# Optimization experiments

Hardware: AMD Instinct MI355X
Metric: run time of the kernel (lower is better)

The kernel has to match this reference:

```python
import jax, jax.numpy as jnp
import numpy as np

N, NFEAT, NHID, NCLASS, NLAYERS = 10000, 512, 256, 40, 8
LAMDA, ALPHA = 0.5, 0.1
EDGE_P = 0.003  # avg degree ~30


def setup_inputs() -> dict:
    key = jax.random.key(0)
    ks = jax.random.split(key, 8)
    x = jax.random.normal(ks[0], (N, NFEAT), dtype=jnp.float32)
    # binary adjacency with zero diagonal (normalize_adj asserts diag==0)
    adj = (jax.random.uniform(ks[1], (N, N)) < EDGE_P).astype(jnp.float32)
    adj = adj * (1.0 - jnp.eye(N, dtype=jnp.float32))
    # GraphConvolution.reset_parameters: uniform(-1/sqrt(out), 1/sqrt(out))
    s = 1.0 / np.sqrt(NHID)
    conv_w = jax.random.uniform(ks[2], (NLAYERS, NHID, NHID), jnp.float32, -s, s)
    s0 = 1.0 / np.sqrt(NFEAT)
    w0 = jax.random.uniform(ks[3], (NFEAT, NHID), jnp.float32, -s0, s0)
    b0 = jax.random.uniform(ks[4], (NHID,), jnp.float32, -s0, s0)
    s1 = 1.0 / np.sqrt(NHID)
    w1 = jax.random.uniform(ks[5], (NHID, NCLASS), jnp.float32, -s1, s1)
    b1 = jax.random.uniform(ks[6], (NCLASS,), jnp.float32, -s1, s1)
    return {"x": x, "adj": adj, "w0": w0, "b0": b0, "conv_w": conv_w, "w1": w1, "b1": b1}


def reference(x, adj, w0, b0, conv_w, w1, b1):
    n = adj.shape[0]
    # normalize_adj: A_hat = A + I; D^{-1/2} A_hat D^{-1/2}
    a_hat = adj + jnp.eye(n, dtype=adj.dtype)
    d_inv_sqrt = jax.lax.rsqrt(jnp.sum(a_hat, axis=1))
    a_norm = a_hat * d_inv_sqrt[:, None] * d_inv_sqrt[None, :]

    # dropout is a no-op in eval mode
    h0 = jax.nn.relu(x @ w0 + b0)  # [N, NHID]
    thetas = jnp.log(LAMDA / jnp.arange(1, NLAYERS + 1, dtype=jnp.float32) + 1.0)

    def step(h, wt):
        w, theta = wt
        hi = a_norm @ h                              # aggregation
        support = (1.0 - ALPHA) * hi + ALPHA * h0    # initial-residual mix (variant=False: r = support)
        out = theta * (support @ w) + (1.0 - theta) * support
        return jax.nn.relu(out), None

    h, _ = jax.lax.scan(step, h0, (conv_w, thetas))
    logits = h @ w1 + b1  # [N, NCLASS]
    return jax.nn.log_softmax(logits, axis=1)
```

## Files before the change

kernel.cpp:

```cpp
#include <hip/hip_runtime.h>
#include <math.h>

#define NN 10000
#define NFEAT 512
#define NHID 256
#define NCLASS 40
#define NLAYERS 8
#define MAXDEG 96

#define CVX_BLOCKS 5000
#define PW_BLOCKS  2560
#define PE_BLOCKS  3750

typedef __attribute__((ext_vector_type(8))) short bf16x8;
typedef __attribute__((ext_vector_type(4))) float floatx4;
typedef __attribute__((ext_vector_type(2))) float floatx2;
typedef __attribute__((ext_vector_type(4))) unsigned short ushort4v;

__device__ __forceinline__ unsigned short f2bf(float f) {
    union { float f; unsigned int u; } v; v.f = f;
    unsigned int r = v.u + 0x7fffu + ((v.u >> 16) & 1u);
    return (unsigned short)(r >> 16);
}
__device__ __forceinline__ float bf2f(unsigned short h) {
    union { unsigned int u; float f; } v; v.u = ((unsigned int)h) << 16;
    return v.f;
}
__device__ __forceinline__ unsigned char f2fp8(float f) {
    return (unsigned char)(__builtin_amdgcn_cvt_pk_fp8_f32(f, f, 0, false) & 0xFF);
}

__global__ __launch_bounds__(256) void build_graph(const float* __restrict__ adj,
                                                   int* __restrict__ cnt,
                                                   int* __restrict__ ell,
                                                   float* __restrict__ dinv) {
    int i = blockIdx.x;
    __shared__ int scnt;
    if (threadIdx.x == 0) scnt = 0;
    __syncthreads();
    const float4* row = (const float4*)(adj + (size_t)i * NN);
    const int nv = NN / 4;
    int* erow = ell + (size_t)i * MAXDEG;
    for (int f = threadIdx.x; f < nv; f += 256) {
        float4 v = row[f];
        if (v.x != 0.0f) { int s = atomicAdd(&scnt, 1); if (s < MAXDEG) erow[s] = 4*f + 0; }
        if (v.y != 0.0f) { int s = atomicAdd(&scnt, 1); if (s < MAXDEG) erow[s] = 4*f + 1; }
        if (v.z != 0.0f) { int s = atomicAdd(&scnt, 1); if (s < MAXDEG) erow[s] = 4*f + 2; }
        if (v.w != 0.0f) { int s = atomicAdd(&scnt, 1); if (s < MAXDEG) erow[s] = 4*f + 3; }
    }
    __syncthreads();
    if (threadIdx.x == 0) {
        int c = scnt;
        cnt[i] = (c < MAXDEG) ? c : MAXDEG;
        dinv[i] = rsqrtf(1.0f + (float)c);
    }
}

__global__ __launch_bounds__(256) void prep_all(const float* __restrict__ x,
                                                unsigned short* __restrict__ xb,
                                                const float* __restrict__ w0,
                                                const float* __restrict__ cw,
                                                unsigned short* __restrict__ w0t,
                                                unsigned short* __restrict__ Mt,
                                                const int* __restrict__ ell,
                                                const int* __restrict__ cnt,
                                                const float* __restrict__ dinv,
                                                int2* __restrict__ es) {
    int b = blockIdx.x, t = threadIdx.x;
    if (b < CVX_BLOCKS) {
        int idx = b * 256 + t;
        float4 v = ((const float4*)x)[idx];
        ushort4v o;
        o.x = f2bf(v.x); o.y = f2bf(v.y); o.z = f2bf(v.z); o.w = f2bf(v.w);
        ((ushort4v*)xb)[idx] = o;
    } else if (b < CVX_BLOCKS + PW_BLOCKS) {
        int idx = (b - CVX_BLOCKS) * 256 + t;
        if (idx < 131072) {
            int n = idx >> 9, k = idx & 511;
            w0t[idx] = f2bf(w0[(size_t)k * 256 + n]);
        } else {
            int j = idx - 131072;
            int l = j >> 16;
            int r = j & 65535;
            int n = r >> 8, k = r & 255;
            float theta = logf(0.5f / (float)(l + 1) + 1.0f);
            float v = theta * cw[(size_t)l * 65536 + (size_t)k * 256 + n];
            if (k == n) v += 1.0f - theta;
            Mt[j] = f2bf(v);
        }
    } else {
        int idx = (b - CVX_BLOCKS - PW_BLOCKS) * 256 + t;
        if (idx >= NN * MAXDEG) return;
        int i = idx / MAXDEG, e = idx % MAXDEG;
        int2 v; v.x = 0; v.y = 0;
        if (e < cnt[i]) {
            int j = ell[idx];
            v.x = j; v.y = __float_as_int(dinv[j]);
        }
        es[idx] = v;
    }
}

__global__ __launch_bounds__(512, 4) void gemm0_mfma(const unsigned short* __restrict__ xb,
                                                     const unsigned short* __restrict__ w0t,
                                                     const float* __restrict__ b0,
                                                     unsigned short* __restrict__ h0b,
                                                     unsigned char* __restrict__ h8o) {
    int t = threadIdx.x, wv = t >> 6, lane = t & 63;
    int lrow = lane & 15, quad = lane >> 4;
    int r0 = blockIdx.x * 16;

    bf16x8 a[16];
    const unsigned short* arow = xb + (size_t)(r0 + lrow) * NFEAT + quad * 8;
    #pragma unroll
    for (int f = 0; f < 16; ++f)
        a[f] = *(const bf16x8*)(arow + f * 32);

    #pragma unroll 1
    for (int n = 0; n < 2; ++n) {
        int nt = wv * 2 + n;
        floatx4 acc = {0.f, 0.f, 0.f, 0.f};
        const unsigned short* wrow = w0t + (size_t)(nt * 16 + lrow) * NFEAT + quad * 8;
        #pragma unroll
        for (int f = 0; f < 16; ++f) {
            bf16x8 b = *(const bf16x8*)(wrow + f * 32);
            acc = __builtin_amdgcn_mfma_f32_16x16x32_bf16(a[f], b, acc, 0, 0, 0);
        }
        int col = nt * 16 + lrow;
        float bias = b0[col];
        #pragma unroll
        for (int r = 0; r < 4; ++r) {
            int row = r0 + quad * 4 + r;
            unsigned short bv = f2bf(fmaxf(acc[r] + bias, 0.f));
            h0b[(size_t)row * NHID + col] = bv;
            h8o[(size_t)row * NHID + col] = f2fp8(bf2f(bv));
        }
    }
}

__device__ __forceinline__ void load_hg(const int2* __restrict__ e0r,
                                        const int2* __restrict__ e1r,
                                        const unsigned int* __restrict__ h8,
                                        int lane, int base,
                                        unsigned int (&x0)[4], unsigned int (&x1)[4],
                                        float (&s0)[4], float (&s1)[4]) {
    #pragma unroll
    for (int u = 0; u < 4; ++u) {
        int2 p = e0r[base + u];
        int2 q = e1r[base + u];
        s0[u] = __int_as_float(p.y);
        s1[u] = __int_as_float(q.y);
        x0[u] = h8[(size_t)p.x * 64 + lane];
        x1[u] = h8[(size_t)q.x * 64 + lane];
    }
}

__device__ __forceinline__ void proc_hg(const unsigned int (&x0)[4],
                                        const unsigned int (&x1)[4],
                                        const float (&s0)[4], const float (&s1)[4],
                                        float4& a0, float4& a1) {
    #pragma unroll
    for (int u = 0; u < 4; ++u) {
        floatx2 lo = __builtin_amdgcn_cvt_pk_f32_fp8(x0[u], false);
        floatx2 hi = __builtin_amdgcn_cvt_pk_f32_fp8(x0[u], true);
        a0.x = fmaf(s0[u], lo.x, a0.x);
        a0.y = fmaf(s0[u], lo.y, a0.y);
        a0.z = fmaf(s0[u], hi.x, a0.z);
        a0.w = fmaf(s0[u], hi.y, a0.w);
        lo = __builtin_amdgcn_cvt_pk_f32_fp8(x1[u], false);
        hi = __builtin_amdgcn_cvt_pk_f32_fp8(x1[u], true);
        a1.x = fmaf(s1[u], lo.x, a1.x);
        a1.y = fmaf(s1[u], lo.y, a1.y);
        a1.z = fmaf(s1[u], hi.x, a1.z);
        a1.w = fmaf(s1[u], hi.y, a1.w);
    }
}

template<bool LAST>
__global__ __launch_bounds__(512, 6) void layer_fused(const unsigned int* __restrict__ h8,
                                                      const unsigned short* __restrict__ h0b,
                                                      const float* __restrict__ dinv,
                                                      const int* __restrict__ cnt,
                                                      const int2* __restrict__ es,
                                                      const unsigned short* __restrict__ Mt,
                                                      const float* __restrict__ w1,
                                                      const float* __restrict__ b1,
                                                      unsigned char* __restrict__ h8_out,
                                                      float* __restrict__ out) {
    __shared__ unsigned short supb[16][264];
    __shared__ float hs[LAST ? 16 * 264 : 4];

    int t = threadIdx.x;
    int wv = __builtin_amdgcn_readfirstlane(t >> 6);
    int lane = t & 63;
    int r0 = blockIdx.x * 16;

    int lr0 = wv * 2, lr1 = lr0 + 1;
    int i0 = r0 + lr0, i1 = r0 + lr1;

    unsigned int su0 = h8[(size_t)i0 * 64 + lane];
    unsigned int su1 = h8[(size_t)i1 * 64 + lane];
    ushort4v h0v0 = ((const ushort4v*)h0b)[(size_t)i0 * 64 + lane];
    ushort4v h0v1 = ((const ushort4v*)h0b)[(size_t)i1 * 64 + lane];

    float di0 = dinv[i0], di1 = dinv[i1];
    int dA = (cnt[i0] + 7) & ~7, dB = (cnt[i1] + 7) & ~7;
    int dm = dA > dB ? dA : dB;
    const int2* e0r = es + (size_t)i0 * MAXDEG;
    const int2* e1r = es + (size_t)i1 * MAXDEG;

    floatx2 slo = __builtin_amdgcn_cvt_pk_f32_fp8(su0, false);
    floatx2 shi = __builtin_amdgcn_cvt_pk_f32_fp8(su0, true);
    float4 a0, a1;
    a0.x = di0 * slo.x; a0.y = di0 * slo.y; a0.z = di0 * shi.x; a0.w = di0 * shi.y;
    slo = __builtin_amdgcn_cvt_pk_f32_fp8(su1, false);
    shi = __builtin_amdgcn_cvt_pk_f32_fp8(su1, true);
    a1.x = di1 * slo.x; a1.y = di1 * slo.y; a1.z = di1 * shi.x; a1.w = di1 * shi.y;

    unsigned int xA0[4], xA1[4], xB0[4], xB1[4];
    float sA0[4], sA1[4], sB0[4], sB1[4];
    int nh = dm >> 2;
    if (nh > 0) {
        load_hg(e0r, e1r, h8, lane, 0, xA0, xA1, sA0, sA1);
        bool useA = true;
        #pragma unroll 1
        for (int g = 1; g < nh; ++g) {
            if (useA) {
                load_hg(e0r, e1r, h8, lane, g << 2, xB0, xB1, sB0, sB1);
                proc_hg(xA0, xA1, sA0, sA1, a0, a1);
            } else {
                load_hg(e0r, e1r, h8, lane, g << 2, xA0, xA1, sA0, sA1);
                proc_hg(xB0, xB1, sB0, sB1, a0, a1);
            }
            useA = !useA;
        }
        if (useA) proc_hg(xA0, xA1, sA0, sA1, a0, a1);
        else      proc_hg(xB0, xB1, sB0, sB1, a0, a1);
    }

    ushort4v ob;
    ob.x = f2bf(0.9f * (di0 * a0.x) + 0.1f * bf2f(h0v0.x));
    ob.y = f2bf(0.9f * (di0 * a0.y) + 0.1f * bf2f(h0v0.y));
    ob.z = f2bf(0.9f * (di0 * a0.z) + 0.1f * bf2f(h0v0.z));
    ob.w = f2bf(0.9f * (di0 * a0.w) + 0.1f * bf2f(h0v0.w));
    *(ushort4v*)&supb[lr0][4 * lane] = ob;
    ob.x = f2bf(0.9f * (di1 * a1.x) + 0.1f * bf2f(h0v1.x));
    ob.y = f2bf(0.9f * (di1 * a1.y) + 0.1f * bf2f(h0v1.y));
    ob.z = f2bf(0.9f * (di1 * a1.z) + 0.1f * bf2f(h0v1.z));
    ob.w = f2bf(0.9f * (di1 * a1.w) + 0.1f * bf2f(h0v1.w));
    *(ushort4v*)&supb[lr1][4 * lane] = ob;
    __syncthreads();

    int lrow = lane & 15, quad = lane >> 4;
    bf16x8 a[8];
    #pragma unroll
    for (int f = 0; f < 8; ++f)
        a[f] = *(const bf16x8*)&supb[lrow][quad * 8 + f * 32];

    #pragma unroll 1
    for (int n = 0; n < 2; ++n) {
        int nt = wv * 2 + n;
        floatx4 acc = {0.f, 0.f, 0.f, 0.f};
        const unsigned short* wrow = Mt + (size_t)(nt * 16 + lrow) * NHID + quad * 8;
        #pragma unroll
        for (int f = 0; f < 8; ++f) {
            bf16x8 b = *(const bf16x8*)(wrow + f * 32);
            acc = __builtin_amdgcn_mfma_f32_16x16x32_bf16(a[f], b, acc, 0, 0, 0);
        }
        int col = nt * 16 + lrow;
        #pragma unroll
        for (int r = 0; r < 4; ++r) {
            int lr2 = quad * 4 + r;
            float o = fmaxf(acc[r], 0.f);
            if (LAST) {
                hs[lr2 * 264 + col] = o;
            } else {
                h8_out[(size_t)(r0 + lr2) * NHID + col] = f2fp8(o);
            }
        }
    }

    if (LAST) {
        __syncthreads();
        #pragma unroll 1
        for (int rr = 0; rr < 2; ++rr) {
            int lr = wv * 2 + rr;
            const float* hr = hs + lr * 264;
            float logit = -1e30f;
            if (lane < NCLASS) {
                float acc = b1[lane];
                #pragma unroll 8
                for (int k = 0; k < NHID; ++k)
                    acc = fmaf(hr[k], w1[k * NCLASS + lane], acc);
                logit = acc;
            }
            float m = logit;
            #pragma unroll
            for (int off = 32; off > 0; off >>= 1)
                m = fmaxf(m, __shfl_xor(m, off, 64));
            float e = (lane < NCLASS) ? expf(logit - m) : 0.0f;
            float ssum = e;
            #pragma unroll
            for (int off = 32; off > 0; off >>= 1)
                ssum += __shfl_xor(ssum, off, 64);
            float lse = m + logf(ssum);
            if (lane < NCLASS)
                out[(size_t)(r0 + lr) * NCLASS + lane] = logit - lse;
        }
    }
}

extern "C" void kernel_launch(void* const* d_in, const int* in_sizes, int n_in,
                              void* d_out, int out_size, void* d_ws, size_t ws_size,
                              hipStream_t stream) {
    const float* x      = (const float*)d_in[0];
    const float* adj    = (const float*)d_in[1];
    const float* w0     = (const float*)d_in[2];
    const float* b0     = (const float*)d_in[3];
    const float* conv_w = (const float*)d_in[4];
    const float* w1     = (const float*)d_in[5];
    const float* b1     = (const float*)d_in[6];
    float* out = (float*)d_out;

    char* ws = (char*)d_ws;
    size_t off = 0;
    auto alloc = [&](size_t bytes) -> void* {
        void* p = ws + off;
        off = (off + bytes + 255) & ~(size_t)255;
        return p;
    };
    float*          dinv  = (float*)alloc((size_t)NN * 4);
    int*            cnt   = (int*)  alloc((size_t)NN * 4);
    int*            ell   = (int*)  alloc((size_t)NN * MAXDEG * 4);
    int2*           es    = (int2*) alloc((size_t)NN * MAXDEG * 8);
    unsigned short* xb    = (unsigned short*)alloc((size_t)NN * NFEAT * 2);
    unsigned short* w0t   = (unsigned short*)alloc((size_t)NFEAT * NHID * 2);
    unsigned short* Mt    = (unsigned short*)alloc((size_t)NLAYERS * NHID * NHID * 2);
    unsigned short* h0b   = (unsigned short*)alloc((size_t)NN * NHID * 2);
    unsigned int*   h08   = (unsigned int*)alloc((size_t)NN * NHID);
    unsigned int*   hP8   = (unsigned int*)alloc((size_t)NN * NHID);
    unsigned int*   hQ8   = (unsigned int*)alloc((size_t)NN * NHID);

    build_graph<<<NN, 256, 0, stream>>>(adj, cnt, ell, dinv);
    prep_all<<<CVX_BLOCKS + PW_BLOCKS + PE_BLOCKS, 256, 0, stream>>>(
        x, xb, w0, conv_w, w0t, Mt, ell, cnt, dinv, es);
    gemm0_mfma<<<NN / 16, 512, 0, stream>>>(xb, w0t, b0, h0b, (unsigned char*)h08);

    const unsigned int* hc8 = h08;
    for (int l = 0; l < NLAYERS; ++l) {
        unsigned int* nxt = (l & 1) ? hQ8 : hP8;
        const unsigned short* wt = Mt + (size_t)l * NHID * NHID;
        if (l == NLAYERS - 1)
            layer_fused<true><<<NN / 16, 512, 0, stream>>>(hc8, h0b, dinv, cnt, es, wt, w1, b1, nullptr, out);
        else
            layer_fused<false><<<NN / 16, 512, 0, stream>>>(hc8, h0b, dinv, cnt, es, wt, nullptr, nullptr, (unsigned char*)nxt, nullptr);
        hc8 = nxt;
    }
}
```

Measured before the change: 777.7 us.

## Stage neighbor gathers through LDS via global_load_lds and merge prep kernels

The neighbor aggregation in each layer now issues chunks of 16 neighbor-row gathers per row directly into per-wave LDS staging with global_load_lds, waits once, then accumulates from LDS. This replaces the register double-buffered gather loop and is meant to raise memory-level parallelism. The graph build, casting and weight-prep kernels are merged into one launch, and edge-list packing is merged with the first GEMM, cutting the launch count from three to two. Costs include a full vmcnt(0) stall per chunk with no overlap between chunks, more LDS per block, and a lower occupancy hint (6 to 4).

```diff
diff --git a/kernel.cpp b/kernel.cpp
--- a/kernel.cpp
+++ b/kernel.cpp
@@ -7,10 +7,13 @@
 #define NCLASS 40
 #define NLAYERS 8
 #define MAXDEG 96
-
+#define CH 16
+
+#define BG_BLOCKS  10000
 #define CVX_BLOCKS 5000
 #define PW_BLOCKS  2560
-#define PE_BLOCKS  3750
+#define G0_BLOCKS  625
+#define PE_BLOCKS  1875
 
 typedef __attribute__((ext_vector_type(8))) short bf16x8;
 typedef __attribute__((ext_vector_type(4))) float floatx4;
@@ -30,51 +33,52 @@
     return (unsigned char)(__builtin_amdgcn_cvt_pk_fp8_f32(f, f, 0, false) & 0xFF);
 }
 
-__global__ __launch_bounds__(256) void build_graph(const float* __restrict__ adj,
-                                                   int* __restrict__ cnt,
-                                                   int* __restrict__ ell,
-                                                   float* __restrict__ dinv) {
-    int i = blockIdx.x;
-    __shared__ int scnt;
-    if (threadIdx.x == 0) scnt = 0;
-    __syncthreads();
-    const float4* row = (const float4*)(adj + (size_t)i * NN);
-    const int nv = NN / 4;
-    int* erow = ell + (size_t)i * MAXDEG;
-    for (int f = threadIdx.x; f < nv; f += 256) {
-        float4 v = row[f];
-        if (v.x != 0.0f) { int s = atomicAdd(&scnt, 1); if (s < MAXDEG) erow[s] = 4*f + 0; }
-        if (v.y != 0.0f) { int s = atomicAdd(&scnt, 1); if (s < MAXDEG) erow[s] = 4*f + 1; }
-        if (v.z != 0.0f) { int s = atomicAdd(&scnt, 1); if (s < MAXDEG) erow[s] = 4*f + 2; }
-        if (v.w != 0.0f) { int s = atomicAdd(&scnt, 1); if (s < MAXDEG) erow[s] = 4*f + 3; }
-    }
-    __syncthreads();
-    if (threadIdx.x == 0) {
-        int c = scnt;
-        cnt[i] = (c < MAXDEG) ? c : MAXDEG;
-        dinv[i] = rsqrtf(1.0f + (float)c);
-    }
-}
-
-__global__ __launch_bounds__(256) void prep_all(const float* __restrict__ x,
-                                                unsigned short* __restrict__ xb,
-                                                const float* __restrict__ w0,
-                                                const float* __restrict__ cw,
-                                                unsigned short* __restrict__ w0t,
-                                                unsigned short* __restrict__ Mt,
-                                                const int* __restrict__ ell,
-                                                const int* __restrict__ cnt,
-                                                const float* __restrict__ dinv,
-                                                int2* __restrict__ es) {
+__device__ __forceinline__ void glds4(const unsigned int* g, unsigned int* l) {
+    __builtin_amdgcn_global_load_lds(
+        (const __attribute__((address_space(1))) unsigned int*)g,
+        (__attribute__((address_space(3))) unsigned int*)l,
+        4, 0, 0);
+}
+
+__global__ __launch_bounds__(256) void mega_prep(const float* __restrict__ adj,
+                                                 int* __restrict__ cnt,
+                                                 int* __restrict__ ell,
+                                                 float* __restrict__ dinv,
+                                                 const float* __restrict__ x,
+                                                 unsigned short* __restrict__ xb,
+                                                 const float* __restrict__ w0,
+                                                 const float* __restrict__ cw,
+                                                 unsigned short* __restrict__ w0t,
+                                                 unsigned short* __restrict__ Mt) {
     int b = blockIdx.x, t = threadIdx.x;
-    if (b < CVX_BLOCKS) {
-        int idx = b * 256 + t;
+    if (b < BG_BLOCKS) {
+        int i = b;
+        __shared__ int scnt;
+        if (t == 0) scnt = 0;
+        __syncthreads();
+        const float4* row = (const float4*)(adj + (size_t)i * NN);
+        int* erow = ell + (size_t)i * MAXDEG;
+        for (int f = t; f < NN / 4; f += 256) {
+            float4 v = row[f];
+            if (v.x != 0.0f) { int s = atomicAdd(&scnt, 1); if (s < MAXDEG) erow[s] = 4*f + 0; }
+            if (v.y != 0.0f) { int s = atomicAdd(&scnt, 1); if (s < MAXDEG) erow[s] = 4*f + 1; }
+            if (v.z != 0.0f) { int s = atomicAdd(&scnt, 1); if (s < MAXDEG) erow[s] = 4*f + 2; }
+            if (v.w != 0.0f) { int s = atomicAdd(&scnt, 1); if (s < MAXDEG) erow[s] = 4*f + 3; }
+        }
+        __syncthreads();
+        if (t == 0) {
+            int c = scnt;
+            cnt[i] = (c < MAXDEG) ? c : MAXDEG;
+            dinv[i] = rsqrtf(1.0f + (float)c);
+        }
+    } else if (b < BG_BLOCKS + CVX_BLOCKS) {
+        int idx = (b - BG_BLOCKS) * 256 + t;
         float4 v = ((const float4*)x)[idx];
         ushort4v o;
         o.x = f2bf(v.x); o.y = f2bf(v.y); o.z = f2bf(v.z); o.w = f2bf(v.w);
         ((ushort4v*)xb)[idx] = o;
-    } else if (b < CVX_BLOCKS + PW_BLOCKS) {
-        int idx = (b - CVX_BLOCKS) * 256 + t;
+    } else {
+        int idx = (b - BG_BLOCKS - CVX_BLOCKS) * 256 + t;
         if (idx < 131072) {
             int n = idx >> 9, k = idx & 511;
             w0t[idx] = f2bf(w0[(size_t)k * 256 + n]);
@@ -88,8 +92,21 @@
             if (k == n) v += 1.0f - theta;
             Mt[j] = f2bf(v);
         }
-    } else {
-        int idx = (b - CVX_BLOCKS - PW_BLOCKS) * 256 + t;
+    }
+}
+
+__global__ __launch_bounds__(512, 4) void gemm0_prep(const unsigned short* __restrict__ xb,
+                                                     const unsigned short* __restrict__ w0t,
+                                                     const float* __restrict__ b0,
+                                                     unsigned short* __restrict__ h0b,
+                                                     unsigned char* __restrict__ h8o,
+                                                     const int* __restrict__ ell,
+                                                     const int* __restrict__ cnt,
+                                                     const float* __restrict__ dinv,
+                                                     int2* __restrict__ es) {
+    int b = blockIdx.x, t = threadIdx.x;
+    if (b >= G0_BLOCKS) {
+        int idx = (b - G0_BLOCKS) * 512 + t;
         if (idx >= NN * MAXDEG) return;
         int i = idx / MAXDEG, e = idx % MAXDEG;
         int2 v; v.x = 0; v.y = 0;
@@ -98,17 +115,11 @@
             v.x = j; v.y = __float_as_int(dinv[j]);
         }
         es[idx] = v;
-    }
-}
-
-__global__ __launch_bounds__(512, 4) void gemm0_mfma(const unsigned short* __restrict__ xb,
-                                                     const unsigned short* __restrict__ w0t,
-                                                     const float* __restrict__ b0,
-                                                     unsigned short* __restrict__ h0b,
-                                                     unsigned char* __restrict__ h8o) {
-    int t = threadIdx.x, wv = t >> 6, lane = t & 63;
+        return;
+    }
+    int wv = t >> 6, lane = t & 63;
     int lrow = lane & 15, quad = lane >> 4;
-    int r0 = blockIdx.x * 16;
+    int r0 = b * 16;
 
     bf16x8 a[16];
     const unsigned short* arow = xb + (size_t)(r0 + lrow) * NFEAT + quad * 8;
@@ -123,8 +134,8 @@
         const unsigned short* wrow = w0t + (size_t)(nt * 16 + lrow) * NFEAT + quad * 8;
         #pragma unroll
         for (int f = 0; f < 16; ++f) {
-            bf16x8 b = *(const bf16x8*)(wrow + f * 32);
-            acc = __builtin_amdgcn_mfma_f32_16x16x32_bf16(a[f], b, acc, 0, 0, 0);
+            bf16x8 bb = *(const bf16x8*)(wrow + f * 32);
+            acc = __builtin_amdgcn_mfma_f32_16x16x32_bf16(a[f], bb, acc, 0, 0, 0);
         }
         int col = nt * 16 + lrow;
         float bias = b0[col];
@@ -138,46 +149,8 @@
     }
 }
 
-__device__ __forceinline__ void load_hg(const int2* __restrict__ e0r,
-                                        const int2* __restrict__ e1r,
-                                        const unsigned int* __restrict__ h8,
-                                        int lane, int base,
-                                        unsigned int (&x0)[4], unsigned int (&x1)[4],
-                                        float (&s0)[4], float (&s1)[4]) {
-    #pragma unroll
-    for (int u = 0; u < 4; ++u) {
-        int2 p = e0r[base + u];
-        int2 q = e1r[base + u];
-        s0[u] = __int_as_float(p.y);
-        s1[u] = __int_as_float(q.y);
-        x0[u] = h8[(size_t)p.x * 64 + lane];
-        x1[u] = h8[(size_t)q.x * 64 + lane];
-    }
-}
-
-__device__ __forceinline__ void proc_hg(const unsigned int (&x0)[4],
-                                        const unsigned int (&x1)[4],
-                                        const float (&s0)[4], const float (&s1)[4],
-                                        float4& a0, float4& a1) {
-    #pragma unroll
-    for (int u = 0; u < 4; ++u) {
-        floatx2 lo = __builtin_amdgcn_cvt_pk_f32_fp8(x0[u], false);
-        floatx2 hi = __builtin_amdgcn_cvt_pk_f32_fp8(x0[u], true);
-        a0.x = fmaf(s0[u], lo.x, a0.x);
-        a0.y = fmaf(s0[u], lo.y, a0.y);
-        a0.z = fmaf(s0[u], hi.x, a0.z);
-        a0.w = fmaf(s0[u], hi.y, a0.w);
-        lo = __builtin_amdgcn_cvt_pk_f32_fp8(x1[u], false);
-        hi = __builtin_amdgcn_cvt_pk_f32_fp8(x1[u], true);
-        a1.x = fmaf(s1[u], lo.x, a1.x);
-        a1.y = fmaf(s1[u], lo.y, a1.y);
-        a1.z = fmaf(s1[u], hi.x, a1.z);
-        a1.w = fmaf(s1[u], hi.y, a1.w);
-    }
-}
-
 template<bool LAST>
-__global__ __launch_bounds__(512, 6) void layer_fused(const unsigned int* __restrict__ h8,
+__global__ __launch_bounds__(512, 4) void layer_fused(const unsigned int* __restrict__ h8,
                                                       const unsigned short* __restrict__ h0b,
                                                       const float* __restrict__ dinv,
                                                       const int* __restrict__ cnt,
@@ -188,7 +161,8 @@
                                                       unsigned char* __restrict__ h8_out,
                                                       float* __restrict__ out) {
     __shared__ unsigned short supb[16][264];
-    __shared__ float hs[LAST ? 16 * 264 : 4];
+    __shared__ unsigned int stage[8][2 * CH * 64];
+    float* hs = (float*)&stage[0][0];
 
     int t = threadIdx.x;
     int wv = __builtin_amdgcn_readfirstlane(t >> 6);
@@ -206,6 +180,7 @@
     float di0 = dinv[i0], di1 = dinv[i1];
     int dA = (cnt[i0] + 7) & ~7, dB = (cnt[i1] + 7) & ~7;
     int dm = dA > dB ? dA : dB;
+    int dm16 = (dm + CH - 1) & ~(CH - 1);
     const int2* e0r = es + (size_t)i0 * MAXDEG;
     const int2* e1r = es + (size_t)i1 * MAXDEG;
 
@@ -217,25 +192,42 @@
     shi = __builtin_amdgcn_cvt_pk_f32_fp8(su1, true);
     a1.x = di1 * slo.x; a1.y = di1 * slo.y; a1.z = di1 * shi.x; a1.w = di1 * shi.y;
 
-    unsigned int xA0[4], xA1[4], xB0[4], xB1[4];
-    float sA0[4], sA1[4], sB0[4], sB1[4];
-    int nh = dm >> 2;
-    if (nh > 0) {
-        load_hg(e0r, e1r, h8, lane, 0, xA0, xA1, sA0, sA1);
-        bool useA = true;
-        #pragma unroll 1
-        for (int g = 1; g < nh; ++g) {
-            if (useA) {
-                load_hg(e0r, e1r, h8, lane, g << 2, xB0, xB1, sB0, sB1);
-                proc_hg(xA0, xA1, sA0, sA1, a0, a1);
-            } else {
-                load_hg(e0r, e1r, h8, lane, g << 2, xA0, xA1, sA0, sA1);
-                proc_hg(xB0, xB1, sB0, sB1, a0, a1);
-            }
-            useA = !useA;
-        }
-        if (useA) proc_hg(xA0, xA1, sA0, sA1, a0, a1);
-        else      proc_hg(xB0, xB1, sB0, sB1, a0, a1);
+    unsigned int* sl0 = &stage[wv][0];
+    unsigned int* sl1 = &stage[wv][CH * 64];
+
+    #pragma unroll 1
+    for (int c0 = 0; c0 < dm16; c0 += CH) {
+        float sc0[CH], sc1[CH];
+        #pragma unroll
+        for (int u = 0; u < CH; ++u) {
+            int2 p = e0r[c0 + u];
+            int2 q = e1r[c0 + u];
+            sc0[u] = __int_as_float(p.y);
+            sc1[u] = __int_as_float(q.y);
+            glds4(h8 + (size_t)p.x * 64 + lane, sl0 + u * 64);
+            glds4(h8 + (size_t)q.x * 64 + lane, sl1 + u * 64);
+        }
+        asm volatile("s_waitcnt vmcnt(0)" ::: "memory");
+        #pragma unroll
+        for (int u = 0; u < CH; ++u) {
+            unsigned int x0 = sl0[u * 64 + lane];
+            floatx2 lo = __builtin_amdgcn_cvt_pk_f32_fp8(x0, false);
+            floatx2 hi = __builtin_amdgcn_cvt_pk_f32_fp8(x0, true);
+            a0.x = fmaf(sc0[u], lo.x, a0.x);
+            a0.y = fmaf(sc0[u], lo.y, a0.y);
+            a0.z = fmaf(sc0[u], hi.x, a0.z);
+            a0.w = fmaf(sc0[u], hi.y, a0.w);
+        }
+        #pragma unroll
+        for (int u = 0; u < CH; ++u) {
+            unsigned int x1 = sl1[u * 64 + lane];
+            floatx2 lo = __builtin_amdgcn_cvt_pk_f32_fp8(x1, false);
+            floatx2 hi = __builtin_amdgcn_cvt_pk_f32_fp8(x1, true);
+            a1.x = fmaf(sc1[u], lo.x, a1.x);
+            a1.y = fmaf(sc1[u], lo.y, a1.y);
+            a1.z = fmaf(sc1[u], hi.x, a1.z);
+            a1.w = fmaf(sc1[u], hi.y, a1.w);
+        }
     }
 
     ushort4v ob;
@@ -264,8 +256,8 @@
         const unsigned short* wrow = Mt + (size_t)(nt * 16 + lrow) * NHID + quad * 8;
         #pragma unroll
         for (int f = 0; f < 8; ++f) {
-            bf16x8 b = *(const bf16x8*)(wrow + f * 32);
-            acc = __builtin_amdgcn_mfma_f32_16x16x32_bf16(a[f], b, acc, 0, 0, 0);
+            bf16x8 bb = *(const bf16x8*)(wrow + f * 32);
+            acc = __builtin_amdgcn_mfma_f32_16x16x32_bf16(a[f], bb, acc, 0, 0, 0);
         }
         int col = nt * 16 + lrow;
         #pragma unroll
@@ -341,10 +333,10 @@
     unsigned int*   hP8   = (unsigned int*)alloc((size_t)NN * NHID);
     unsigned int*   hQ8   = (unsigned int*)alloc((size_t)NN * NHID);
 
-    build_graph<<<NN, 256, 0, stream>>>(adj, cnt, ell, dinv);
-    prep_all<<<CVX_BLOCKS + PW_BLOCKS + PE_BLOCKS, 256, 0, stream>>>(
-        x, xb, w0, conv_w, w0t, Mt, ell, cnt, dinv, es);
-    gemm0_mfma<<<NN / 16, 512, 0, stream>>>(xb, w0t, b0, h0b, (unsigned char*)h08);
+    mega_prep<<<BG_BLOCKS + CVX_BLOCKS + PW_BLOCKS, 256, 0, stream>>>(
+        adj, cnt, ell, dinv, x, xb, w0, conv_w, w0t, Mt);
+    gemm0_prep<<<G0_BLOCKS + PE_BLOCKS, 512, 0, stream>>>(
+        xb, w0t, b0, h0b, (unsigned char*)h08, ell, cnt, dinv, es);
 
     const unsigned int* hc8 = h08;
     for (int l = 0; l < NLAYERS; ++l) {
```

Result: slower. 805.9 us (+3.6%).

## Sort rows by degree and give each wave one row in layer kernels

Applied to the files above, without the earlier changes.

Adds a degree histogram and a counting-sort permutation so that each 16-row block of a layer kernel processes rows with similar neighbour counts. Each layer block now uses 1024 threads with one wave per row instead of two rows per wave. The neighbour gather walks two halves of the edge list with 8-wide loads in place of a double-buffered 4-wide pipeline. Outputs are scattered back through the permutation. The aim is to cut wave divergence and imbalance from irregular degrees, at the cost of an extra kernel, atomics, scattered output writes and a tight launch bound that may force register spills.

```diff
diff --git a/kernel.cpp b/kernel.cpp
--- a/kernel.cpp
+++ b/kernel.cpp
@@ -7,10 +7,12 @@
 #define NCLASS 40
 #define NLAYERS 8
 #define MAXDEG 96
+#define NBINS 97
 
 #define CVX_BLOCKS 5000
 #define PW_BLOCKS  2560
 #define PE_BLOCKS  3750
+#define RK_BLOCKS  40
 
 typedef __attribute__((ext_vector_type(8))) short bf16x8;
 typedef __attribute__((ext_vector_type(4))) float floatx4;
@@ -30,18 +32,24 @@
     return (unsigned char)(__builtin_amdgcn_cvt_pk_fp8_f32(f, f, 0, false) & 0xFF);
 }
 
+__global__ __launch_bounds__(256) void zero_bins(int* __restrict__ hist,
+                                                 int* __restrict__ cur) {
+    int t = threadIdx.x;
+    if (t < NBINS) { hist[t] = 0; cur[t] = 0; }
+}
+
 __global__ __launch_bounds__(256) void build_graph(const float* __restrict__ adj,
                                                    int* __restrict__ cnt,
                                                    int* __restrict__ ell,
-                                                   float* __restrict__ dinv) {
+                                                   float* __restrict__ dinv,
+                                                   int* __restrict__ hist) {
     int i = blockIdx.x;
     __shared__ int scnt;
     if (threadIdx.x == 0) scnt = 0;
     __syncthreads();
     const float4* row = (const float4*)(adj + (size_t)i * NN);
-    const int nv = NN / 4;
     int* erow = ell + (size_t)i * MAXDEG;
-    for (int f = threadIdx.x; f < nv; f += 256) {
+    for (int f = threadIdx.x; f < NN / 4; f += 256) {
         float4 v = row[f];
         if (v.x != 0.0f) { int s = atomicAdd(&scnt, 1); if (s < MAXDEG) erow[s] = 4*f + 0; }
         if (v.y != 0.0f) { int s = atomicAdd(&scnt, 1); if (s < MAXDEG) erow[s] = 4*f + 1; }
@@ -51,8 +59,10 @@
     __syncthreads();
     if (threadIdx.x == 0) {
         int c = scnt;
-        cnt[i] = (c < MAXDEG) ? c : MAXDEG;
-        dinv[i] = rsqrtf(1.0f + (float)c);
+        c = (c < MAXDEG) ? c : MAXDEG;
+        cnt[i] = c;
+        dinv[i] = rsqrtf(1.0f + (float)scnt);
+        atomicAdd(&hist[c], 1);
     }
 }
 
@@ -65,7 +75,11 @@
                                                 const int* __restrict__ ell,
                                                 const int* __restrict__ cnt,
                                                 const float* __restrict__ dinv,
-                                                int2* __restrict__ es) {
+                                                int2* __restrict__ es,
+                                                const int* __restrict__ hist,
+                                                int* __restrict__ cur,
+                                                int* __restrict__ P) {
+    __shared__ int pre[NBINS];
     int b = blockIdx.x, t = threadIdx.x;
     if (b < CVX_BLOCKS) {
         int idx = b * 256 + t;
@@ -88,7 +102,7 @@
             if (k == n) v += 1.0f - theta;
             Mt[j] = f2bf(v);
         }
-    } else {
+    } else if (b < CVX_BLOCKS + PW_BLOCKS + PE_BLOCKS) {
         int idx = (b - CVX_BLOCKS - PW_BLOCKS) * 256 + t;
         if (idx >= NN * MAXDEG) return;
         int i = idx / MAXDEG, e = idx % MAXDEG;
@@ -98,6 +112,18 @@
             v.x = j; v.y = __float_as_int(dinv[j]);
         }
         es[idx] = v;
+    } else {
+        int idx = (b - CVX_BLOCKS - PW_BLOCKS - PE_BLOCKS) * 256 + t;
+        if (t == 0) {
+            int s = 0;
+            for (int k = NBINS - 1; k >= 0; --k) { pre[k] = s; s += hist[k]; }
+        }
+        __syncthreads();
+        if (idx < NN) {
+            int d = cnt[idx];
+            int r = pre[d] + atomicAdd(&cur[d], 1);
+            P[r] = idx;
+        }
     }
 }
 
@@ -123,8 +149,8 @@
         const unsigned short* wrow = w0t + (size_t)(nt * 16 + lrow) * NFEAT + quad * 8;
         #pragma unroll
         for (int f = 0; f < 16; ++f) {
-            bf16x8 b = *(const bf16x8*)(wrow + f * 32);
-            acc = __builtin_amdgcn_mfma_f32_16x16x32_bf16(a[f], b, acc, 0, 0, 0);
+            bf16x8 bb = *(const bf16x8*)(wrow + f * 32);
+            acc = __builtin_amdgcn_mfma_f32_16x16x32_bf16(a[f], bb, acc, 0, 0, 0);
         }
         int col = nt * 16 + lrow;
         float bias = b0[col];
@@ -138,175 +164,138 @@
     }
 }
 
-__device__ __forceinline__ void load_hg(const int2* __restrict__ e0r,
-                                        const int2* __restrict__ e1r,
-                                        const unsigned int* __restrict__ h8,
-                                        int lane, int base,
-                                        unsigned int (&x0)[4], unsigned int (&x1)[4],
-                                        float (&s0)[4], float (&s1)[4]) {
-    #pragma unroll
-    for (int u = 0; u < 4; ++u) {
-        int2 p = e0r[base + u];
-        int2 q = e1r[base + u];
-        s0[u] = __int_as_float(p.y);
-        s1[u] = __int_as_float(q.y);
-        x0[u] = h8[(size_t)p.x * 64 + lane];
-        x1[u] = h8[(size_t)q.x * 64 + lane];
-    }
-}
-
-__device__ __forceinline__ void proc_hg(const unsigned int (&x0)[4],
-                                        const unsigned int (&x1)[4],
-                                        const float (&s0)[4], const float (&s1)[4],
-                                        float4& a0, float4& a1) {
-    #pragma unroll
-    for (int u = 0; u < 4; ++u) {
-        floatx2 lo = __builtin_amdgcn_cvt_pk_f32_fp8(x0[u], false);
-        floatx2 hi = __builtin_amdgcn_cvt_pk_f32_fp8(x0[u], true);
-        a0.x = fmaf(s0[u], lo.x, a0.x);
-        a0.y = fmaf(s0[u], lo.y, a0.y);
-        a0.z = fmaf(s0[u], hi.x, a0.z);
-        a0.w = fmaf(s0[u], hi.y, a0.w);
-        lo = __builtin_amdgcn_cvt_pk_f32_fp8(x1[u], false);
-        hi = __builtin_amdgcn_cvt_pk_f32_fp8(x1[u], true);
-        a1.x = fmaf(s1[u], lo.x, a1.x);
-        a1.y = fmaf(s1[u], lo.y, a1.y);
-        a1.z = fmaf(s1[u], hi.x, a1.z);
-        a1.w = fmaf(s1[u], hi.y, a1.w);
-    }
-}
-
 template<bool LAST>
-__global__ __launch_bounds__(512, 6) void layer_fused(const unsigned int* __restrict__ h8,
-                                                      const unsigned short* __restrict__ h0b,
-                                                      const float* __restrict__ dinv,
-                                                      const int* __restrict__ cnt,
-                                                      const int2* __restrict__ es,
-                                                      const unsigned short* __restrict__ Mt,
-                                                      const float* __restrict__ w1,
-                                                      const float* __restrict__ b1,
-                                                      unsigned char* __restrict__ h8_out,
-                                                      float* __restrict__ out) {
+__global__ __launch_bounds__(1024, 8) void layer_fused(const unsigned int* __restrict__ h8,
+                                                       const unsigned short* __restrict__ h0b,
+                                                       const float* __restrict__ dinv,
+                                                       const int* __restrict__ cnt,
+                                                       const int2* __restrict__ es,
+                                                       const int* __restrict__ P,
+                                                       const unsigned short* __restrict__ Mt,
+                                                       const float* __restrict__ w1,
+                                                       const float* __restrict__ b1,
+                                                       unsigned char* __restrict__ h8_out,
+                                                       float* __restrict__ out) {
     __shared__ unsigned short supb[16][264];
     __shared__ float hs[LAST ? 16 * 264 : 4];
+    __shared__ int sp[16];
 
     int t = threadIdx.x;
     int wv = __builtin_amdgcn_readfirstlane(t >> 6);
     int lane = t & 63;
     int r0 = blockIdx.x * 16;
-
-    int lr0 = wv * 2, lr1 = lr0 + 1;
-    int i0 = r0 + lr0, i1 = r0 + lr1;
-
-    unsigned int su0 = h8[(size_t)i0 * 64 + lane];
-    unsigned int su1 = h8[(size_t)i1 * 64 + lane];
-    ushort4v h0v0 = ((const ushort4v*)h0b)[(size_t)i0 * 64 + lane];
-    ushort4v h0v1 = ((const ushort4v*)h0b)[(size_t)i1 * 64 + lane];
-
-    float di0 = dinv[i0], di1 = dinv[i1];
-    int dA = (cnt[i0] + 7) & ~7, dB = (cnt[i1] + 7) & ~7;
-    int dm = dA > dB ? dA : dB;
-    const int2* e0r = es + (size_t)i0 * MAXDEG;
-    const int2* e1r = es + (size_t)i1 * MAXDEG;
-
-    floatx2 slo = __builtin_amdgcn_cvt_pk_f32_fp8(su0, false);
-    floatx2 shi = __builtin_amdgcn_cvt_pk_f32_fp8(su0, true);
-    float4 a0, a1;
-    a0.x = di0 * slo.x; a0.y = di0 * slo.y; a0.z = di0 * shi.x; a0.w = di0 * shi.y;
-    slo = __builtin_amdgcn_cvt_pk_f32_fp8(su1, false);
-    shi = __builtin_amdgcn_cvt_pk_f32_fp8(su1, true);
-    a1.x = di1 * slo.x; a1.y = di1 * slo.y; a1.z = di1 * shi.x; a1.w = di1 * shi.y;
-
-    unsigned int xA0[4], xA1[4], xB0[4], xB1[4];
-    float sA0[4], sA1[4], sB0[4], sB1[4];
-    int nh = dm >> 2;
-    if (nh > 0) {
-        load_hg(e0r, e1r, h8, lane, 0, xA0, xA1, sA0, sA1);
-        bool useA = true;
-        #pragma unroll 1
-        for (int g = 1; g < nh; ++g) {
-            if (useA) {
-                load_hg(e0r, e1r, h8, lane, g << 2, xB0, xB1, sB0, sB1);
-                proc_hg(xA0, xA1, sA0, sA1, a0, a1);
-            } else {
-                load_hg(e0r, e1r, h8, lane, g << 2, xA0, xA1, sA0, sA1);
-                proc_hg(xB0, xB1, sB0, sB1, a0, a1);
+    if (t < 16) sp[t] = P[r0 + t];
+
+    int i = P[r0 + wv];
+    unsigned int su = h8[(size_t)i * 64 + lane];
+    ushort4v h0v = ((const ushort4v*)h0b)[(size_t)i * 64 + lane];
+    float di = dinv[i];
+    int d = cnt[i];
+    int ng  = ((d + 7) & ~7) >> 3;
+    int nlo = (ng + 1) >> 1, nhi = ng >> 1;
+    const int2* erL = es + (size_t)i * MAXDEG;
+    const int2* erH = erL + (size_t)nlo * 8;
+
+    floatx2 slo = __builtin_amdgcn_cvt_pk_f32_fp8(su, false);
+    floatx2 shi = __builtin_amdgcn_cvt_pk_f32_fp8(su, true);
+    float4 aL, aH;
+    aL.x = di * slo.x; aL.y = di * slo.y; aL.z = di * shi.x; aL.w = di * shi.y;
+    aH.x = 0.f; aH.y = 0.f; aH.z = 0.f; aH.w = 0.f;
+
+    #pragma unroll 1
+    for (int g = 0; g < nlo; ++g) {
+        unsigned int xL[8], xH[8];
+        float sL[8], sH[8];
+        bool hi = (g < nhi);
+        #pragma unroll
+        for (int u = 0; u < 8; ++u) {
+            int2 p = erL[g * 8 + u];
+            sL[u] = __int_as_float(p.y);
+            xL[u] = h8[(size_t)p.x * 64 + lane];
+        }
+        if (hi) {
+            #pragma unroll
+            for (int u = 0; u < 8; ++u) {
+                int2 q = erH[g * 8 + u];
+                sH[u] = __int_as_float(q.y);
+                xH[u] = h8[(size_t)q.x * 64 + lane];
             }
-            useA = !useA;
-        }
-        if (useA) proc_hg(xA0, xA1, sA0, sA1, a0, a1);
-        else      proc_hg(xB0, xB1, sB0, sB1, a0, a1);
+        }
+        #pragma unroll
+        for (int u = 0; u < 8; ++u) {
+            floatx2 lo = __builtin_amdgcn_cvt_pk_f32_fp8(xL[u], false);
+            floatx2 h2 = __builtin_amdgcn_cvt_pk_f32_fp8(xL[u], true);
+            aL.x = fmaf(sL[u], lo.x, aL.x);
+            aL.y = fmaf(sL[u], lo.y, aL.y);
+            aL.z = fmaf(sL[u], h2.x, aL.z);
+            aL.w = fmaf(sL[u], h2.y, aL.w);
+        }
+        if (hi) {
+            #pragma unroll
+            for (int u = 0; u < 8; ++u) {
+                floatx2 lo = __builtin_amdgcn_cvt_pk_f32_fp8(xH[u], false);
+                floatx2 h2 = __builtin_amdgcn_cvt_pk_f32_fp8(xH[u], true);
+                aH.x = fmaf(sH[u], lo.x, aH.x);
+                aH.y = fmaf(sH[u], lo.y, aH.y);
+                aH.z = fmaf(sH[u], h2.x, aH.z);
+                aH.w = fmaf(sH[u], h2.y, aH.w);
+            }
+        }
     }
 
     ushort4v ob;
-    ob.x = f2bf(0.9f * (di0 * a0.x) + 0.1f * bf2f(h0v0.x));
-    ob.y = f2bf(0.9f * (di0 * a0.y) + 0.1f * bf2f(h0v0.y));
-    ob.z = f2bf(0.9f * (di0 * a0.z) + 0.1f * bf2f(h0v0.z));
-    ob.w = f2bf(0.9f * (di0 * a0.w) + 0.1f * bf2f(h0v0.w));
-    *(ushort4v*)&supb[lr0][4 * lane] = ob;
-    ob.x = f2bf(0.9f * (di1 * a1.x) + 0.1f * bf2f(h0v1.x));
-    ob.y = f2bf(0.9f * (di1 * a1.y) + 0.1f * bf2f(h0v1.y));
-    ob.z = f2bf(0.9f * (di1 * a1.z) + 0.1f * bf2f(h0v1.z));
-    ob.w = f2bf(0.9f * (di1 * a1.w) + 0.1f * bf2f(h0v1.w));
-    *(ushort4v*)&supb[lr1][4 * lane] = ob;
+    ob.x = f2bf(0.9f * (di * (aL.x + aH.x)) + 0.1f * bf2f(h0v.x));
+    ob.y = f2bf(0.9f * (di * (aL.y + aH.y)) + 0.1f * bf2f(h0v.y));
+    ob.z = f2bf(0.9f * (di * (aL.z + aH.z)) + 0.1f * bf2f(h0v.z));
+    ob.w = f2bf(0.9f * (di * (aL.w + aH.w)) + 0.1f * bf2f(h0v.w));
+    *(ushort4v*)&supb[wv][4 * lane] = ob;
     __syncthreads();
 
     int lrow = lane & 15, quad = lane >> 4;
-    bf16x8 a[8];
+    bf16x8 afr[8];
     #pragma unroll
     for (int f = 0; f < 8; ++f)
-        a[f] = *(const bf16x8*)&supb[lrow][quad * 8 + f * 32];
-
-    #pragma unroll 1
-    for (int n = 0; n < 2; ++n) {
-        int nt = wv * 2 + n;
-        floatx4 acc = {0.f, 0.f, 0.f, 0.f};
-        const unsigned short* wrow = Mt + (size_t)(nt * 16 + lrow) * NHID + quad * 8;
-        #pragma unroll
-        for (int f = 0; f < 8; ++f) {
-            bf16x8 b = *(const bf16x8*)(wrow + f * 32);
-            acc = __builtin_amdgcn_mfma_f32_16x16x32_bf16(a[f], b, acc, 0, 0, 0);
-        }
-        int col = nt * 16 + lrow;
-        #pragma unroll
-        for (int r = 0; r < 4; ++r) {
-            int lr2 = quad * 4 + r;
-            float o = fmaxf(acc[r], 0.f);
-            if (LAST) {
-                hs[lr2 * 264 + col] = o;
-            } else {
-                h8_out[(size_t)(r0 + lr2) * NHID + col] = f2fp8(o);
-            }
-        }
+        afr[f] = *(const bf16x8*)&supb[lrow][quad * 8 + f * 32];
+
+    floatx4 acc = {0.f, 0.f, 0.f, 0.f};
+    const unsigned short* wrow = Mt + (size_t)(wv * 16 + lrow) * NHID + quad * 8;
+    #pragma unroll
+    for (int f = 0; f < 8; ++f) {
+        bf16x8 bb = *(const bf16x8*)(wrow + f * 32);
+        acc = __builtin_amdgcn_mfma_f32_16x16x32_bf16(afr[f], bb, acc, 0, 0, 0);
+    }
+    int col = wv * 16 + lrow;
+    #pragma unroll
+    for (int r = 0; r < 4; ++r) {
+        int lr2 = quad * 4 + r;
+        float o = fmaxf(acc[r], 0.f);
+        if (LAST) hs[lr2 * 264 + col] = o;
+        else      h8_out[(size_t)sp[lr2] * NHID + col] = f2fp8(o);
     }
 
     if (LAST) {
         __syncthreads();
-        #pragma unroll 1
-        for (int rr = 0; rr < 2; ++rr) {
-            int lr = wv * 2 + rr;
-            const float* hr = hs + lr * 264;
-            float logit = -1e30f;
-            if (lane < NCLASS) {
-                float acc = b1[lane];
-                #pragma unroll 8
-                for (int k = 0; k < NHID; ++k)
-                    acc = fmaf(hr[k], w1[k * NCLASS + lane], acc);
-                logit = acc;
-            }
-            float m = logit;
-            #pragma unroll
-            for (int off = 32; off > 0; off >>= 1)
-                m = fmaxf(m, __shfl_xor(m, off, 64));
-            float e = (lane < NCLASS) ? expf(logit - m) : 0.0f;
-            float ssum = e;
-            #pragma unroll
-            for (int off = 32; off > 0; off >>= 1)
-                ssum += __shfl_xor(ssum, off, 64);
-            float lse = m + logf(ssum);
-            if (lane < NCLASS)
-                out[(size_t)(r0 + lr) * NCLASS + lane] = logit - lse;
-        }
+        const float* hr = hs + wv * 264;
+        float logit = -1e30f;
+        if (lane < NCLASS) {
+            float a2 = b1[lane];
+            #pragma unroll 8
+            for (int k = 0; k < NHID; ++k)
+                a2 = fmaf(hr[k], w1[k * NCLASS + lane], a2);
+            logit = a2;
+        }
+        float m = logit;
+        #pragma unroll
+        for (int off = 32; off > 0; off >>= 1)
+            m = fmaxf(m, __shfl_xor(m, off, 64));
+        float e = (lane < NCLASS) ? expf(logit - m) : 0.0f;
+        float ssum = e;
+        #pragma unroll
+        for (int off = 32; off > 0; off >>= 1)
+            ssum += __shfl_xor(ssum, off, 64);
+        float lse = m + logf(ssum);
+        if (lane < NCLASS)
+            out[(size_t)sp[wv] * NCLASS + lane] = logit - lse;
     }
 }
 
@@ -340,10 +329,14 @@
     unsigned int*   h08   = (unsigned int*)alloc((size_t)NN * NHID);
     unsigned int*   hP8   = (unsigned int*)alloc((size_t)NN * NHID);
     unsigned int*   hQ8   = (unsigned int*)alloc((size_t)NN * NHID);
-
-    build_graph<<<NN, 256, 0, stream>>>(adj, cnt, ell, dinv);
-    prep_all<<<CVX_BLOCKS + PW_BLOCKS + PE_BLOCKS, 256, 0, stream>>>(
-        x, xb, w0, conv_w, w0t, Mt, ell, cnt, dinv, es);
+    int*            hist  = (int*)  alloc(NBINS * 4);
+    int*            curb  = (int*)  alloc(NBINS * 4);
+    int*            P     = (int*)  alloc((size_t)NN * 4);
+
+    zero_bins<<<1, 256, 0, stream>>>(hist, curb);
+    build_graph<<<NN, 256, 0, stream>>>(adj, cnt, ell, dinv, hist);
+    prep_all<<<CVX_BLOCKS + PW_BLOCKS + PE_BLOCKS + RK_BLOCKS, 256, 0, stream>>>(
+        x, xb, w0, conv_w, w0t, Mt, ell, cnt, dinv, es, hist, curb, P);
     gemm0_mfma<<<NN / 16, 512, 0, stream>>>(xb, w0t, b0, h0b, (unsigned char*)h08);
 
     const unsigned int* hc8 = h08;
@@ -351,9 +344,9 @@
         unsigned int* nxt = (l & 1) ? hQ8 : hP8;
         const unsigned short* wt = Mt + (size_t)l * NHID * NHID;
         if (l == NLAYERS - 1)
-            layer_fused<true><<<NN / 16, 512, 0, stream>>>(hc8, h0b, dinv, cnt, es, wt, w1, b1, nullptr, out);
+            layer_fused<true><<<NN / 16, 1024, 0, stream>>>(hc8, h0b, dinv, cnt, es, P, wt, w1, b1, nullptr, out);
         else
-            layer_fused<false><<<NN / 16, 512, 0, stream>>>(hc8, h0b, dinv, cnt, es, wt, nullptr, nullptr, (unsigned char*)nxt, nullptr);
+            layer_fused<false><<<NN / 16, 1024, 0, stream>>>(hc8, h0b, dinv, cnt, es, P, wt, nullptr, nullptr, (unsigned char*)nxt, nullptr);
         hc8 = nxt;
     }
 }
```

Result: slower. 808.3 us (+3.9%).
